# Performance work log

Measured on AMD Instinct MI355X. Metric: run time of the kernel, lower is better.

The kernel has to match this reference:

```python
import jax, jax.numpy as jnp
import numpy as np

B, S, D, H = 2, 2048, 1024, 16
DH = D // H
EPS = 1e-5


def layer_norm(x, g, b):
    # OpenAI-style LN: epsilon inside the sqrt
    u = jnp.mean(x, axis=-1, keepdims=True)
    s = jnp.mean((x - u) ** 2, axis=-1, keepdims=True)
    return g * ((x - u) / jnp.sqrt(s + EPS)) + b


def setup_inputs() -> dict:
    key = jax.random.key(0)
    ks = jax.random.split(key, 8)
    std = 0.002  # Conv1D init std
    return {
        "x": jax.random.normal(ks[0], (B, S, D), dtype=jnp.float32),
        "mask": jnp.ones((B, S), dtype=jnp.bool_),
        "Wqkv": jax.random.normal(ks[1], (D, 3 * D), dtype=jnp.float32) * std,
        "bqkv": jnp.zeros((3 * D,), dtype=jnp.float32),
        "Wvw": jax.random.normal(ks[2], (D, D), dtype=jnp.float32) * std,
        "bvw": jnp.zeros((D,), dtype=jnp.float32),
        "g1": jnp.ones((D,), dtype=jnp.float32),
        "b1": jnp.zeros((D,), dtype=jnp.float32),
        "WA": jax.random.normal(ks[3], (D, 4 * D), dtype=jnp.float32) * std,
        "bA": jnp.zeros((4 * D,), dtype=jnp.float32),
        "WB": jax.random.normal(ks[4], (4 * D, D), dtype=jnp.float32) * std,
        "bB": jnp.zeros((D,), dtype=jnp.float32),
        "g2": jnp.ones((D,), dtype=jnp.float32),
        "b2": jnp.zeros((D,), dtype=jnp.float32),
    }


def reference(x, mask, Wqkv, bqkv, Wvw, bvw, g1, b1, WA, bA, WB, bB, g2, b2):
    maskf = mask.astype(x.dtype)                       # [B,S]
    x = x * maskf[:, :, None]
    # --- multi-head attention ---
    qkv = (x @ Wqkv + bqkv).reshape(B, S, 3, H, DH)    # [B,S,3,H,DH]
    q, k, v = qkv[:, :, 0], qkv[:, :, 1], qkv[:, :, 2]
    w = jnp.einsum('bshd,bzhd->bhsz', q, k) / jnp.sqrt(jnp.asarray(DH, x.dtype))
    causal = jnp.tril(jnp.ones((S, S), dtype=x.dtype)) # [S,S]
    wholemask = maskf[:, None, None, :] * causal[None, None]  # [B,1,S,S]
    w = w + jnp.log(wholemask)                         # additive log-mask (-inf where masked)
    w = jax.nn.softmax(w, axis=-1)
    vw = jnp.einsum('bhsz,bzhd->bshd', w, v).reshape(B, S, D)
    a = vw @ Wvw + bvw
    # --- residual + LN + MLP + LN ---
    n = layer_norm(x + a, g1, b1)
    m = jax.nn.relu(n @ WA + bA) @ WB + bB
    h = layer_norm(n + m, g2, b2)
    return h
```

## Files before the change

### kernel.cpp

```cpp
#include <hip/hip_runtime.h>
#include <stdint.h>

typedef unsigned short u16;
typedef __attribute__((ext_vector_type(8))) short short8;
typedef __attribute__((ext_vector_type(4))) short short4v;
typedef __attribute__((ext_vector_type(4))) float f32x4;

#define NB 2
#define NS 2048
#define ND 1024
#define NH 16
#define NDH 64
#define NBS (NB*NS)

__device__ __forceinline__ float bf2f(u16 u) {
  union { uint32_t i; float f; } c; c.i = ((uint32_t)u) << 16; return c.f;
}
__device__ __forceinline__ u16 f2bf(float f) {
  union { float f; uint32_t i; } c; c.f = f;
  uint32_t r = (c.i + 0x7fffu + ((c.i >> 16) & 1u)) >> 16;
  return (u16)r;
}

__global__ __launch_bounds__(256)
void k_f32_to_bf16(const float* __restrict__ X, u16* __restrict__ Y, int n4) {
  int i = blockIdx.x * 256 + threadIdx.x;
  if (i >= n4) return;
  float4 v = ((const float4*)X)[i];
  uint2 o;
  o.x = (uint32_t)f2bf(v.x) | ((uint32_t)f2bf(v.y) << 16);
  o.y = (uint32_t)f2bf(v.z) | ((uint32_t)f2bf(v.w) << 16);
  ((uint2*)Y)[i] = o;
}

__global__ __launch_bounds__(256)
void k_transpose_all(const float* __restrict__ Wqkv, const float* __restrict__ Wvw,
                     const float* __restrict__ WA, const float* __restrict__ WB,
                     u16* __restrict__ WqkvT, u16* __restrict__ WvwT,
                     u16* __restrict__ WAT, u16* __restrict__ WBT) {
  __shared__ float tile[32][33];
  int id = blockIdx.x;
  const float* W; u16* WT; int K, N, tid;
  if (id < 3072)      { W = Wqkv; WT = WqkvT; K = 1024; N = 3072; tid = id; }
  else if (id < 4096) { W = Wvw;  WT = WvwT;  K = 1024; N = 1024; tid = id - 3072; }
  else if (id < 8192) { W = WA;   WT = WAT;   K = 1024; N = 4096; tid = id - 4096; }
  else                { W = WB;   WT = WBT;   K = 4096; N = 1024; tid = id - 8192; }
  const int ntx = N >> 5;
  const int n0 = (tid % ntx) << 5, k0 = (tid / ntx) << 5;
  const int tx = threadIdx.x & 31, ty = threadIdx.x >> 5;
  #pragma unroll
  for (int j = 0; j < 4; ++j)
    tile[ty + 8*j][tx] = W[(size_t)(k0 + ty + 8*j) * N + (n0 + tx)];
  __syncthreads();
  const int r = threadIdx.x >> 3;
  const int c4 = (threadIdx.x & 7) * 4;
  short4v o;
  #pragma unroll
  for (int i = 0; i < 4; ++i) o[i] = (short)f2bf(tile[c4 + i][r]);
  *(short4v*)(WT + (size_t)(n0 + r) * K + k0 + c4) = o;
}

__global__ __launch_bounds__(256)
void k_vt(const u16* __restrict__ qkv, u16* __restrict__ Vt) {
  __shared__ u16 tile[64][72];
  const int zb = blockIdx.x;
  const int bh = blockIdx.y;
  const int b = bh >> 4, h = bh & 15;
  const int t = threadIdx.x;
  const int r = t >> 2, seg = (t & 3) * 16;
  const u16* src = qkv + ((size_t)(b * NS + zb * 64 + r)) * 3072 + 2048 + h * 64 + seg;
  *(short8*)(&tile[r][seg])     = *(const short8*)(src);
  *(short8*)(&tile[r][seg + 8]) = *(const short8*)(src + 8);
  __syncthreads();
  const int dh = t >> 2, zs = (t & 3) * 16;
  short8 o0, o1;
  #pragma unroll
  for (int i = 0; i < 8; ++i) o0[i] = (short)tile[zs + i][dh];
  #pragma unroll
  for (int i = 0; i < 8; ++i) o1[i] = (short)tile[zs + 8 + i][dh];
  u16* dst = Vt + (size_t)(bh * 64 + dh) * NS + zb * 64 + zs;
  *(short8*)(dst)     = o0;
  *(short8*)(dst + 8) = o1;
}

__device__ __forceinline__ void gload_lds16(const void* g, void* l) {
  __builtin_amdgcn_global_load_lds(
      (const __attribute__((address_space(1))) void*)(void*)(uintptr_t)g,
      (__attribute__((address_space(3))) void*)l, 16, 0, 0);
}

template<bool OUT_BF16, bool RELU>
__global__ __launch_bounds__(256)
void k_gemm_bt(const u16* __restrict__ A, const u16* __restrict__ BT,
               const float* __restrict__ bias, void* __restrict__ C,
               int M, int N, int Kstride, int Klen, size_t zCstride)
{
  __shared__ u16 As[128 * 64];
  __shared__ u16 Bs[128 * 64];
  const int t = threadIdx.x, wave = t >> 6, lane = t & 63;
  const int m0 = blockIdx.y * 128, n0 = blockIdx.x * 128;
  const int wr = wave >> 1, wc = wave & 1;
  const int koff = blockIdx.z * Klen;
  A  += koff;
  BT += koff;

  f32x4 acc[4][4] = {};

  int srow[4], scol[4];
  #pragma unroll
  for (int p = 0; p < 4; ++p) {
    int o = p * 4096 + wave * 1024 + lane * 16;
    int r = o >> 7;
    int cb = o & 127;
    srow[p] = r;
    scol[p] = (cb ^ ((r & 7) << 4)) >> 1;
  }

  const int nkt = Klen >> 6;
  for (int kt = 0; kt < nkt; ++kt) {
    const int k0 = kt << 6;
    #pragma unroll
    for (int p = 0; p < 4; ++p) {
      const u16* srcA = A  + (size_t)(m0 + srow[p]) * Kstride + k0 + scol[p];
      const u16* srcB = BT + (size_t)(n0 + srow[p]) * Kstride + k0 + scol[p];
      gload_lds16(srcA, (char*)As + p * 4096 + wave * 1024);
      gload_lds16(srcB, (char*)Bs + p * 4096 + wave * 1024);
    }
    asm volatile("s_waitcnt vmcnt(0)" ::: "memory");
    __syncthreads();

    #pragma unroll
    for (int kk = 0; kk < 2; ++kk) {
      const int cbase = kk * 64 + ((lane >> 4) << 4);
      short8 af[4], bf[4];
      #pragma unroll
      for (int mi = 0; mi < 4; ++mi) {
        int r = wr * 64 + mi * 16 + (lane & 15);
        af[mi] = *(const short8*)((const char*)As + r * 128 + (cbase ^ ((r & 7) << 4)));
      }
      #pragma unroll
      for (int nj = 0; nj < 4; ++nj) {
        int r = wc * 64 + nj * 16 + (lane & 15);
        bf[nj] = *(const short8*)((const char*)Bs + r * 128 + (cbase ^ ((r & 7) << 4)));
      }
      #pragma unroll
      for (int mi = 0; mi < 4; ++mi)
        #pragma unroll
        for (int nj = 0; nj < 4; ++nj)
          acc[mi][nj] = __builtin_amdgcn_mfma_f32_16x16x32_bf16(af[mi], bf[nj], acc[mi][nj], 0, 0, 0);
    }
    __syncthreads();
  }

  const int lr = (lane >> 4) << 2;
  const int lc = lane & 15;
  #pragma unroll
  for (int nj = 0; nj < 4; ++nj) {
    const int col = n0 + wc * 64 + nj * 16 + lc;
    const float bs = bias ? bias[col] : 0.f;
    #pragma unroll
    for (int mi = 0; mi < 4; ++mi) {
      const int row = m0 + wr * 64 + mi * 16 + lr;
      #pragma unroll
      for (int i = 0; i < 4; ++i) {
        float v = acc[mi][nj][i] + bs;
        if (RELU) v = fmaxf(v, 0.f);
        if (OUT_BF16) ((u16*)C)[blockIdx.z * zCstride + (size_t)(row + i) * N + col] = f2bf(v);
        else          ((float*)C)[blockIdx.z * zCstride + (size_t)(row + i) * N + col] = v;
      }
    }
  }
}

__device__ __forceinline__ short8 lds_frag8(const char* base, int row, int kkbyte) {
  return *(const short8*)(base + row * 128 + (kkbyte ^ ((row & 7) << 4)));
}

template<bool OUT_BF16, bool RELU>
__global__ __launch_bounds__(512, 2)
void k_gemm256(const u16* __restrict__ A, const u16* __restrict__ BT,
               const float* __restrict__ bias, void* __restrict__ C,
               int M, int N, int Kstride, int Klen, int nbx,
               size_t zs1, size_t zs2)
{
  extern __shared__ char lds[];
  char* ldsA = lds;
  char* ldsB = lds + 65536;
  const int t = threadIdx.x, wave = t >> 6, lane = t & 63;
  const int lg = lane >> 4, lq = lane & 15;
  const int wr = wave >> 2, wc = wave & 3;

  const int nwg = gridDim.x;
  const int sw = (blockIdx.x & 7) * (nwg >> 3) + (blockIdx.x >> 3);
  const int bx = sw % nbx, by = sw / nbx;
  const int m0 = by * 256, n0 = bx * 256;

  const int koff = blockIdx.z * Klen;
  A  += koff;
  BT += koff;

  const int rr = t >> 3;
  const int scol = ((t & 7) ^ ((t >> 3) & 7)) * 8;
  const u16* Asrc = A  + (size_t)(m0 + rr) * Kstride + scol;
  const u16* Bsrc = BT + (size_t)(n0 + rr) * Kstride + scol;

  const int nkt = Klen >> 6;
  const int nht = nkt << 2;

  f32x4 acc[8][4] = {};
  short8 af[4][2], bf[4][2];

  auto STAGE = [&](int s) {
    if (s < nht) {
      const int tile = s >> 2, part = s & 3, half = part & 1, slot = tile & 1;
      const u16* src = (part < 2 ? Bsrc : Asrc) + (size_t)(half * 128) * Kstride + tile * 64;
      char* d = (part < 2 ? ldsB : ldsA) + slot * 32768 + half * 16384 + wave * 1024;
      gload_lds16(src, d);
      gload_lds16(src + (size_t)64 * Kstride, d + 8192);
    }
  };
  auto RDA = [&](int slot, int mo) {
    const char* base = ldsA + slot * 32768;
    #pragma unroll
    for (int m = 0; m < 4; ++m) {
      const int row = wr * 128 + (mo + m) * 16 + lq;
      af[m][0] = lds_frag8(base, row, lg * 16);
      af[m][1] = lds_frag8(base, row, 64 + lg * 16);
    }
  };
  auto RDB = [&](int slot, int no) {
    const char* base = ldsB + slot * 32768;
    #pragma unroll
    for (int n = 0; n < 2; ++n) {
      const int row = wc * 64 + (no + n) * 16 + lq;
      bf[no + n][0] = lds_frag8(base, row, lg * 16);
      bf[no + n][1] = lds_frag8(base, row, 64 + lg * 16);
    }
  };
  auto MF = [&](int mo, int no) {
    __builtin_amdgcn_s_setprio(1);
    #pragma unroll
    for (int m = 0; m < 4; ++m)
      #pragma unroll
      for (int n = 0; n < 2; ++n) {
        acc[mo + m][no + n] = __builtin_amdgcn_mfma_f32_16x16x32_bf16(af[m][0], bf[no + n][0], acc[mo + m][no + n], 0, 0, 0);
        acc[mo + m][no + n] = __builtin_amdgcn_mfma_f32_16x16x32_bf16(af[m][1], bf[no + n][1], acc[mo + m][no + n], 0, 0, 0);
      }
    __builtin_amdgcn_s_setprio(0);
  };
  #define BAR() asm volatile("s_barrier" ::: "memory")

  #pragma unroll
  for (int s = 0; s < 6; ++s) STAGE(s);
  asm volatile("s_waitcnt vmcnt(4)" ::: "memory");
  __syncthreads();

  const int niter = nkt >> 1;
  #pragma unroll 1
  for (int i = 0; i < niter; ++i) {
    const int bs = 8 * i + 6;
    RDA(0, 0); RDB(0, 0); STAGE(bs + 0);
    BAR(); MF(0, 0); BAR();
    RDB(0, 2); STAGE(bs + 1);
    BAR(); MF(0, 2); BAR();
    RDA(0, 4); STAGE(bs + 2);
    BAR(); MF(4, 0); BAR();
    STAGE(bs + 3);
    if (i == niter - 1) { asm volatile("s_waitcnt vmcnt(0)" ::: "memory"); }
    else                { asm volatile("s_waitcnt vmcnt(4)" ::: "memory"); }
    BAR(); MF(4, 2); BAR();
    RDA(1, 0); RDB(1, 0); STAGE(bs + 4);
    BAR(); MF(0, 0); BAR();
    RDB(1, 2); STAGE(bs + 5);
    BAR(); MF(0, 2); BAR();
    RDA(1, 4); STAGE(bs + 6);
    BAR(); MF(4, 0); BAR();
    STAGE(bs + 7);
    asm volatile("s_waitcnt vmcnt(4)" ::: "memory");
    BAR(); MF(4, 2); BAR();
  }
  #undef BAR

  const size_t zoff = (size_t)(blockIdx.z & 1) * zs1 + (size_t)(blockIdx.z >> 1) * zs2;
  #pragma unroll
  for (int n = 0; n < 4; ++n) {
    const int col = n0 + wc * 64 + n * 16 + lq;
    const float bs = bias ? bias[col] : 0.f;
    #pragma unroll
    for (int m = 0; m < 8; ++m) {
      const int row = m0 + wr * 128 + m * 16 + lg * 4;
      #pragma unroll
      for (int i = 0; i < 4; ++i) {
        float v = acc[m][n][i] + bs;
        if (RELU) v = fmaxf(v, 0.f);
        if (OUT_BF16) ((u16*)C)[zoff + (size_t)(row + i) * N + col] = f2bf(v);
        else          ((float*)C)[zoff + (size_t)(row + i) * N + col] = v;
      }
    }
  }
}

__global__ __launch_bounds__(512)
void k_flash_attn(const u16* __restrict__ qkv, const u16* __restrict__ Vt,
                  u16* __restrict__ vw)
{
  __shared__ u16 Ks[2][64 * 64];
  __shared__ u16 Vts[2][64 * 64];
  __shared__ u16 P_lds[8][16 * 72];

  const int qb = 15 - (int)blockIdx.x;
  const int bh = blockIdx.y;
  const int b = bh >> 4, h = bh & 15;
  const int t = threadIdx.x, wave = t >> 6, lane = t & 63;
  const int lg = lane >> 4, lq = lane & 15;

  const int q0w = qb * 128 + wave * 16;

  const float QSC = 0.18033688f;
  short8 bq[2];
  {
    const u16* qrow = qkv + ((size_t)(b * NS + q0w + lq)) * 3072 + h * 64 + lg * 8;
    short8 r0 = *(const short8*)(qrow);
    short8 r1 = *(const short8*)(qrow + 32);
    union { short8 s; uint32_t u[4]; } o0, o1;
    #pragma unroll
    for (int p = 0; p < 4; ++p) {
      float a0 = bf2f((u16)r0[2*p]) * QSC, a1 = bf2f((u16)r0[2*p+1]) * QSC;
      float c0 = bf2f((u16)r1[2*p]) * QSC, c1 = bf2f((u16)r1[2*p+1]) * QSC;
      asm("v_cvt_pk_bf16_f32 %0, %1, %2" : "=v"(o0.u[p]) : "v"(a0), "v"(a1));
      asm("v_cvt_pk_bf16_f32 %0, %1, %2" : "=v"(o1.u[p]) : "v"(c0), "v"(c1));
    }
    bq[0] = o0.s; bq[1] = o1.s;
  }

  f32x4 o_acc[4] = {};
  float m_run = -1e30f, l_run = 0.f;

  const u16* kbase = qkv + (size_t)b * NS * 3072 + 1024 + h * 64;
  const u16* vtb   = Vt + (size_t)bh * 64 * NS;

  const int so = t * 16;
  const int sr = so >> 7;
  const int scb = (so & 127) ^ ((sr & 7) << 4);
  const int npairs = qb + 1;

  short8 rK0, rK1, rV0, rV1;
  auto LOADP = [&](int z0) {
    rK0 = *(const short8*)(kbase + (size_t)(z0 + sr) * 3072 + (scb >> 1));
    rK1 = *(const short8*)(kbase + (size_t)(z0 + 64 + sr) * 3072 + (scb >> 1));
    rV0 = *(const short8*)(vtb + (size_t)sr * NS + z0 + (scb >> 1));
    rV1 = *(const short8*)(vtb + (size_t)sr * NS + z0 + 64 + (scb >> 1));
  };

  LOADP(0);

  for (int kp = 0; kp < npairs; ++kp) {
    const int z0 = kp * 128;
    asm volatile("s_waitcnt vmcnt(0)" ::: "memory");
    *(short8*)((char*)Ks[0]  + so) = rK0;
    *(short8*)((char*)Ks[1]  + so) = rK1;
    *(short8*)((char*)Vts[0] + so) = rV0;
    *(short8*)((char*)Vts[1] + so) = rV1;
    if (kp + 1 < npairs) LOADP(z0 + 128);
    asm volatile("s_waitcnt lgkmcnt(0)" ::: "memory");
    asm volatile("s_barrier" ::: "memory");

    #pragma unroll
    for (int sub = 0; sub < 2; ++sub) {
      const int zz = z0 + (sub << 6);
      if (zz <= q0w + 15) {
        f32x4 s_acc[4];
        __builtin_amdgcn_s_setprio(1);
        #pragma unroll
        for (int kb = 0; kb < 4; ++kb) {
          const int r = kb * 16 + lq;
          const int sw = (r & 7) << 4;
          short8 ak0 = *(const short8*)((const char*)Ks[sub] + r * 128 + ((lg * 16) ^ sw));
          short8 ak1 = *(const short8*)((const char*)Ks[sub] + r * 128 + ((64 + lg * 16) ^ sw));
          f32x4 zr = {0.f, 0.f, 0.f, 0.f};
          zr = __builtin_amdgcn_mfma_f32_16x16x32_bf16(ak0, bq[0], zr, 0, 0, 0);
          s_acc[kb] = __builtin_amdgcn_mfma_f32_16x16x32_bf16(ak1, bq[1], zr, 0, 0, 0);
        }
        __builtin_amdgcn_s_setprio(0);

        short8 vb[4][2];
        #pragma unroll
        for (int nb = 0; nb < 4; ++nb) {
          const int rv = nb * 16 + lq;
          const int swv = (rv & 7) << 4;
          vb[nb][0] = *(const short8*)((const char*)Vts[sub] + rv * 128 + ((lg * 16) ^ swv));
          vb[nb][1] = *(const short8*)((const char*)Vts[sub] + rv * 128 + ((64 + lg * 16) ^ swv));
        }

        float sv[16];
        #pragma unroll
        for (int kb = 0; kb < 4; ++kb)
          #pragma unroll
          for (int i = 0; i < 4; ++i)
            sv[kb * 4 + i] = s_acc[kb][i];

        if (zz + 63 > q0w) {
          #pragma unroll
          for (int kb = 0; kb < 4; ++kb)
            #pragma unroll
            for (int i = 0; i < 4; ++i)
              if (zz + kb * 16 + lg * 4 + i > q0w + lq) sv[kb * 4 + i] = -1e30f;
        }

        float tm = -1e30f;
        #pragma unroll
        for (int j = 0; j < 16; ++j) tm = fmaxf(tm, sv[j]);
        tm = fmaxf(tm, __shfl_xor(tm, 16));
        tm = fmaxf(tm, __shfl_xor(tm, 32));

        if (!__all(tm <= m_run + 11.5415603f)) {
          const float m_new = fmaxf(m_run, tm);
          const float scl = __builtin_amdgcn_exp2f(m_run - m_new);
          float s0 = __shfl(scl, lg * 4 + 0);
          float s1 = __shfl(scl, lg * 4 + 1);
          float s2 = __shfl(scl, lg * 4 + 2);
          float s3 = __shfl(scl, lg * 4 + 3);
          #pragma unroll
          for (int nb = 0; nb < 4; ++nb) {
            o_acc[nb][0] *= s0; o_acc[nb][1] *= s1;
            o_acc[nb][2] *= s2; o_acc[nb][3] *= s3;
          }
          l_run *= scl;
          m_run = m_new;
        }

        float ts = 0.f;
        #pragma unroll
        for (int j = 0; j < 16; ++j) {
          float p = __builtin_amdgcn_exp2f(sv[j] - m_run);
          sv[j] = p; ts += p;
        }
        ts += __shfl_xor(ts, 16);
        ts += __shfl_xor(ts, 32);
        l_run += ts;

        #pragma unroll
        for (int kb = 0; kb < 4; ++kb) {
          uint32_t w0, w1;
          asm("v_cvt_pk_bf16_f32 %0, %1, %2" : "=v"(w0) : "v"(sv[kb*4+0]), "v"(sv[kb*4+1]));
          asm("v_cvt_pk_bf16_f32 %0, %1, %2" : "=v"(w1) : "v"(sv[kb*4+2]), "v"(sv[kb*4+3]));
          uint32_t* dst = (uint32_t*)&P_lds[wave][lq * 72 + kb * 16 + lg * 4];
          dst[0] = w0; dst[1] = w1;
        }
        short8 pa0 = *(const short8*)(&P_lds[wave][lq * 72 + lg * 8]);
        short8 pa1 = *(const short8*)(&P_lds[wave][lq * 72 + 32 + lg * 8]);

        __builtin_amdgcn_s_setprio(1);
        #pragma unroll
        for (int nb = 0; nb < 4; ++nb) {
          o_acc[nb] = __builtin_amdgcn_mfma_f32_16x16x32_bf16(pa0, vb[nb][0], o_acc[nb], 0, 0, 0);
          o_acc[nb] = __builtin_amdgcn_mfma_f32_16x16x32_bf16(pa1, vb[nb][1], o_acc[nb], 0, 0, 0);
        }
        __builtin_amdgcn_s_setprio(0);
      }
    }
    asm volatile("s_barrier" ::: "memory");
  }

  #pragma unroll
  for (int i = 0; i < 4; ++i) {
    const float rl = 1.0f / __shfl(l_run, lg * 4 + i);
    const int row = q0w + lg * 4 + i;
    #pragma unroll
    for (int nb = 0; nb < 4; ++nb) {
      const int col = h * 64 + nb * 16 + lq;
      vw[((size_t)b * NS + row) * ND + col] = f2bf(o_acc[nb][i] * rl);
    }
  }
}

__global__ __launch_bounds__(256)
void k_add_ln1s(const float* __restrict__ X, const float* __restrict__ P0,
                const float* __restrict__ P1, const float* __restrict__ bias,
                const float* __restrict__ g, const float* __restrict__ beta,
                float* __restrict__ outf, u16* __restrict__ outb)
{
  const int row = blockIdx.x;
  const int t = threadIdx.x;
  const size_t base = (size_t)row * ND;
  float4 u  = ((const float4*)(X + base))[t];
  float4 p0 = ((const float4*)(P0 + base))[t];
  float4 p1 = ((const float4*)(P1 + base))[t];
  float4 bv = ((const float4*)bias)[t];
  float x0 = u.x + p0.x + p1.x + bv.x;
  float x1 = u.y + p0.y + p1.y + bv.y;
  float x2 = u.z + p0.z + p1.z + bv.z;
  float x3 = u.w + p0.w + p1.w + bv.w;
  float s1 = x0 + x1 + x2 + x3;
  float s2 = x0*x0 + x1*x1 + x2*x2 + x3*x3;
  #pragma unroll
  for (int m = 32; m; m >>= 1) { s1 += __shfl_xor(s1, m); s2 += __shfl_xor(s2, m); }
  __shared__ float rs1[4], rs2[4];
  const int wave = t >> 6;
  if ((t & 63) == 0) { rs1[wave] = s1; rs2[wave] = s2; }
  __syncthreads();
  s1 = rs1[0] + rs1[1] + rs1[2] + rs1[3];
  s2 = rs2[0] + rs2[1] + rs2[2] + rs2[3];
  const float mean = s1 * (1.f / ND);
  const float var  = s2 * (1.f / ND) - mean * mean;
  const float rstd = rsqrtf(var + 1e-5f);
  float4 gg = ((const float4*)g)[t];
  float4 bb = ((const float4*)beta)[t];
  float y0 = gg.x * (x0 - mean) * rstd + bb.x;
  float y1 = gg.y * (x1 - mean) * rstd + bb.y;
  float y2 = gg.z * (x2 - mean) * rstd + bb.z;
  float y3 = gg.w * (x3 - mean) * rstd + bb.w;
  ((float4*)(outf + base))[t] = make_float4(y0, y1, y2, y3);
  uint2 ob;
  ob.x = (uint32_t)f2bf(y0) | ((uint32_t)f2bf(y1) << 16);
  ob.y = (uint32_t)f2bf(y2) | ((uint32_t)f2bf(y3) << 16);
  ((uint2*)(outb + base))[t] = ob;
}

__global__ __launch_bounds__(256)
void k_add_ln2b(const float* __restrict__ U,
                const u16* __restrict__ p0, const u16* __restrict__ p1,
                const u16* __restrict__ p2, const u16* __restrict__ p3,
                const float* __restrict__ bias,
                const float* __restrict__ g, const float* __restrict__ beta,
                float* __restrict__ outf)
{
  const int row = blockIdx.x;
  const int t = threadIdx.x;
  const size_t base = (size_t)row * ND;
  float4 u  = ((const float4*)(U + base))[t];
  float4 bv = ((const float4*)bias)[t];
  uint2 a0 = ((const uint2*)(p0 + base))[t];
  uint2 a1 = ((const uint2*)(p1 + base))[t];
  uint2 a2 = ((const uint2*)(p2 + base))[t];
  uint2 a3 = ((const uint2*)(p3 + base))[t];
  float x0 = u.x + bv.x + bf2f((u16)(a0.x)) + bf2f((u16)(a1.x)) + bf2f((u16)(a2.x)) + bf2f((u16)(a3.x));
  float x1 = u.y + bv.y + bf2f((u16)(a0.x >> 16)) + bf2f((u16)(a1.x >> 16)) + bf2f((u16)(a2.x >> 16)) + bf2f((u16)(a3.x >> 16));
  float x2 = u.z + bv.z + bf2f((u16)(a0.y)) + bf2f((u16)(a1.y)) + bf2f((u16)(a2.y)) + bf2f((u16)(a3.y));
  float x3 = u.w + bv.w + bf2f((u16)(a0.y >> 16)) + bf2f((u16)(a1.y >> 16)) + bf2f((u16)(a2.y >> 16)) + bf2f((u16)(a3.y >> 16));
  float s1 = x0 + x1 + x2 + x3;
  float s2 = x0*x0 + x1*x1 + x2*x2 + x3*x3;
  #pragma unroll
  for (int m = 32; m; m >>= 1) { s1 += __shfl_xor(s1, m); s2 += __shfl_xor(s2, m); }
  __shared__ float rs1[4], rs2[4];
  const int wave = t >> 6;
  if ((t & 63) == 0) { rs1[wave] = s1; rs2[wave] = s2; }
  __syncthreads();
  s1 = rs1[0] + rs1[1] + rs1[2] + rs1[3];
  s2 = rs2[0] + rs2[1] + rs2[2] + rs2[3];
  const float mean = s1 * (1.f / ND);
  const float var  = s2 * (1.f / ND) - mean * mean;
  const float rstd = rsqrtf(var + 1e-5f);
  float4 gg = ((const float4*)g)[t];
  float4 bb = ((const float4*)beta)[t];
  float y0 = gg.x * (x0 - mean) * rstd + bb.x;
  float y1 = gg.y * (x1 - mean) * rstd + bb.y;
  float y2 = gg.z * (x2 - mean) * rstd + bb.z;
  float y3 = gg.w * (x3 - mean) * rstd + bb.w;
  ((float4*)(outf + base))[t] = make_float4(y0, y1, y2, y3);
}

__global__ __launch_bounds__(256)
void k_add_ln2(const float* __restrict__ U, const float* __restrict__ P0,
               const float* __restrict__ P1, const float* __restrict__ bias,
               const float* __restrict__ g, const float* __restrict__ beta,
               float* __restrict__ outf)
{
  const int row = blockIdx.x;
  const int t = threadIdx.x;
  const size_t base = (size_t)row * ND;
  float4 u  = ((const float4*)(U + base))[t];
  float4 p0 = ((const float4*)(P0 + base))[t];
  float4 p1 = ((const float4*)(P1 + base))[t];
  float4 bv = ((const float4*)bias)[t];
  float x0 = u.x + p0.x + p1.x + bv.x;
  float x1 = u.y + p0.y + p1.y + bv.y;
  float x2 = u.z + p0.z + p1.z + bv.z;
  float x3 = u.w + p0.w + p1.w + bv.w;
  float s1 = x0 + x1 + x2 + x3;
  float s2 = x0*x0 + x1*x1 + x2*x2 + x3*x3;
  #pragma unroll
  for (int m = 32; m; m >>= 1) { s1 += __shfl_xor(s1, m); s2 += __shfl_xor(s2, m); }
  __shared__ float rs1[4], rs2[4];
  const int wave = t >> 6;
  if ((t & 63) == 0) { rs1[wave] = s1; rs2[wave] = s2; }
  __syncthreads();
  s1 = rs1[0] + rs1[1] + rs1[2] + rs1[3];
  s2 = rs2[0] + rs2[1] + rs2[2] + rs2[3];
  const float mean = s1 * (1.f / ND);
  const float var  = s2 * (1.f / ND) - mean * mean;
  const float rstd = rsqrtf(var + 1e-5f);
  float4 gg = ((const float4*)g)[t];
  float4 bb = ((const float4*)beta)[t];
  float y0 = gg.x * (x0 - mean) * rstd + bb.x;
  float y1 = gg.y * (x1 - mean) * rstd + bb.y;
  float y2 = gg.z * (x2 - mean) * rstd + bb.z;
  float y3 = gg.w * (x3 - mean) * rstd + bb.w;
  ((float4*)(outf + base))[t] = make_float4(y0, y1, y2, y3);
}

extern "C" void kernel_launch(void* const* d_in, const int* in_sizes, int n_in,
                              void* d_out, int out_size, void* d_ws, size_t ws_size,
                              hipStream_t stream) {
  const float* x    = (const float*)d_in[0];
  const float* Wqkv = (const float*)d_in[2];
  const float* bqkv = (const float*)d_in[3];
  const float* Wvw  = (const float*)d_in[4];
  const float* bvw  = (const float*)d_in[5];
  const float* g1   = (const float*)d_in[6];
  const float* b1   = (const float*)d_in[7];
  const float* WA   = (const float*)d_in[8];
  const float* bA   = (const float*)d_in[9];
  const float* WB   = (const float*)d_in[10];
  const float* bB   = (const float*)d_in[11];
  const float* g2   = (const float*)d_in[12];
  const float* b2   = (const float*)d_in[13];
  float* out = (float*)d_out;

  if (ws_size < 100663296) return;
  char* ws = (char*)d_ws;
  u16*  WqkvT = (u16*)(ws + 0);
  u16*  WvwT  = (u16*)(ws + 6291456);
  u16*  WAT   = (u16*)(ws + 8388608);
  u16*  WBT   = (u16*)(ws + 16777216);
  u16*  xb    = (u16*)(ws + 25165824);
  u16*  qkvb  = (u16*)(ws + 33554432);
  u16*  vwb   = (u16*)(ws + 58720256);
  float* pp0  = (float*)(ws + 67108864);
  float* pp1  = (float*)(ws + 83886080);
  float* nf   = (float*)(ws + 83886080);
  u16*  nb    = (u16*)(ws + 25165824);
  u16*  z     = (u16*)(ws + 33554432);
  u16*  Vtb   = (u16*)(ws + 67108864);
  u16*  pb01  = (u16*)(ws + 0);
  u16*  pb23  = (u16*)(ws + 67108864);
  float* pp   = (float*)ws;

  hipError_t e2 = hipFuncSetAttribute((const void*)&k_gemm256<true, true>,
                                      hipFuncAttributeMaxDynamicSharedMemorySize, 131072);
  hipError_t e1 = hipFuncSetAttribute((const void*)&k_gemm256<true, false>,
                                      hipFuncAttributeMaxDynamicSharedMemorySize, 131072);
  const bool use256 = (e1 == hipSuccess) && (e2 == hipSuccess);

  k_f32_to_bf16<<<dim3(NBS * ND / 4 / 256), 256, 0, stream>>>(x, xb, NBS * ND / 4);
  k_transpose_all<<<dim3(12288), 256, 0, stream>>>(Wqkv, Wvw, WA, WB, WqkvT, WvwT, WAT, WBT);

  k_gemm_bt<true, false><<<dim3(3 * ND / 128, NBS / 128, 1), 256, 0, stream>>>(
      xb, WqkvT, bqkv, qkvb, NBS, 3 * ND, ND, ND, 0);

  k_vt<<<dim3(NS / 64, NB * NH), 256, 0, stream>>>(qkvb, Vtb);
  k_flash_attn<<<dim3(NS / 128, NB * NH), 512, 0, stream>>>(qkvb, Vtb, vwb);

  k_gemm_bt<false, false><<<dim3(ND / 128, NBS / 128, 2), 256, 0, stream>>>(
      vwb, WvwT, nullptr, pp0, NBS, ND, ND, ND / 2, (size_t)(pp1 - pp0));

  k_add_ln1s<<<dim3(NBS), 256, 0, stream>>>(x, pp0, pp1, bvw, g1, b1, nf, nb);

  if (use256)
    k_gemm256<true, true><<<dim3(256), 512, 131072, stream>>>(
        nb, WAT, bA, z, NBS, 4 * ND, ND, ND, 16, 0, 0);
  else
    k_gemm_bt<true, true><<<dim3(4 * ND / 128, NBS / 128, 1), 256, 0, stream>>>(
        nb, WAT, bA, z, NBS, 4 * ND, ND, ND, 0);

  if (use256) {
    k_gemm256<true, false><<<dim3(64, 1, 4), 512, 131072, stream>>>(
        z, WBT, nullptr, pb01, NBS, ND, 4 * ND, ND, 4,
        (size_t)4194304, (size_t)(pb23 - pb01));
    k_add_ln2b<<<dim3(NBS), 256, 0, stream>>>(
        nf, pb01, pb01 + 4194304, pb23, pb23 + 4194304, bB, g2, b2, out);
  } else {
    k_gemm_bt<false, false><<<dim3(ND / 128, NBS / 128, 2), 256, 0, stream>>>(
        z, WBT, nullptr, pp, NBS, ND, 4 * ND, 2 * ND, (size_t)16777216);
    k_add_ln2<<<dim3(NBS), 256, 0, stream>>>(nf, pp, pp + 16777216, bB, g2, b2, out);
  }
}
```

Baseline: 232.2 us.

## Merge prep kernels, halve attention block size, store split-K partials in bf16

Combines the x-to-bf16 conversion and weight transpose into one prep launch. The flash attention kernel now uses 64-query blocks of 4 waves, which doubles the grid. Each thread stages twice as much K/V data per iteration. The Wvw split-K partials are written as bf16 instead of fp32 to cut traffic into LN1, at some precision cost. The fallback MLP path now uses four bf16 partials and the shared LN2b kernel.

```diff
diff --git a/kernel.cpp b/kernel.cpp
--- a/kernel.cpp
+++ b/kernel.cpp
@@ -23,23 +23,22 @@
 }
 
 __global__ __launch_bounds__(256)
-void k_f32_to_bf16(const float* __restrict__ X, u16* __restrict__ Y, int n4) {
-  int i = blockIdx.x * 256 + threadIdx.x;
-  if (i >= n4) return;
-  float4 v = ((const float4*)X)[i];
-  uint2 o;
-  o.x = (uint32_t)f2bf(v.x) | ((uint32_t)f2bf(v.y) << 16);
-  o.y = (uint32_t)f2bf(v.z) | ((uint32_t)f2bf(v.w) << 16);
-  ((uint2*)Y)[i] = o;
-}
-
-__global__ __launch_bounds__(256)
-void k_transpose_all(const float* __restrict__ Wqkv, const float* __restrict__ Wvw,
-                     const float* __restrict__ WA, const float* __restrict__ WB,
-                     u16* __restrict__ WqkvT, u16* __restrict__ WvwT,
-                     u16* __restrict__ WAT, u16* __restrict__ WBT) {
+void k_prep(const float* __restrict__ x, u16* __restrict__ xb,
+            const float* __restrict__ Wqkv, const float* __restrict__ Wvw,
+            const float* __restrict__ WA, const float* __restrict__ WB,
+            u16* __restrict__ WqkvT, u16* __restrict__ WvwT,
+            u16* __restrict__ WAT, u16* __restrict__ WBT) {
   __shared__ float tile[32][33];
   int id = blockIdx.x;
+  if (id >= 12288) {
+    int i = (id - 12288) * 256 + threadIdx.x;
+    float4 v = ((const float4*)x)[i];
+    uint2 o;
+    o.x = (uint32_t)f2bf(v.x) | ((uint32_t)f2bf(v.y) << 16);
+    o.y = (uint32_t)f2bf(v.z) | ((uint32_t)f2bf(v.w) << 16);
+    ((uint2*)xb)[i] = o;
+    return;
+  }
   const float* W; u16* WT; int K, N, tid;
   if (id < 3072)      { W = Wqkv; WT = WqkvT; K = 1024; N = 3072; tid = id; }
   else if (id < 4096) { W = Wvw;  WT = WvwT;  K = 1024; N = 1024; tid = id - 3072; }
@@ -300,21 +299,21 @@
   }
 }
 
-__global__ __launch_bounds__(512)
+__global__ __launch_bounds__(256)
 void k_flash_attn(const u16* __restrict__ qkv, const u16* __restrict__ Vt,
                   u16* __restrict__ vw)
 {
   __shared__ u16 Ks[2][64 * 64];
   __shared__ u16 Vts[2][64 * 64];
-  __shared__ u16 P_lds[8][16 * 72];
-
-  const int qb = 15 - (int)blockIdx.x;
+  __shared__ u16 P_lds[4][16 * 72];
+
+  const int qb = 31 - (int)blockIdx.x;
   const int bh = blockIdx.y;
   const int b = bh >> 4, h = bh & 15;
   const int t = threadIdx.x, wave = t >> 6, lane = t & 63;
   const int lg = lane >> 4, lq = lane & 15;
 
-  const int q0w = qb * 128 + wave * 16;
+  const int q0w = qb * 64 + wave * 16;
 
   const float QSC = 0.18033688f;
   short8 bq[2];
@@ -339,17 +338,27 @@
   const u16* kbase = qkv + (size_t)b * NS * 3072 + 1024 + h * 64;
   const u16* vtb   = Vt + (size_t)bh * 64 * NS;
 
-  const int so = t * 16;
+  const int so = t * 32;
   const int sr = so >> 7;
-  const int scb = (so & 127) ^ ((sr & 7) << 4);
-  const int npairs = qb + 1;
-
-  short8 rK0, rK1, rV0, rV1;
+  const int cb = so & 127;
+  const int swz = (sr & 7) << 4;
+  const int sc0 = (cb ^ swz) >> 1;
+  const int sc1 = ((cb + 16) ^ swz) >> 1;
+  const int npairs = (qb >> 1) + 1;
+
+  short8 rg[8];
   auto LOADP = [&](int z0) {
-    rK0 = *(const short8*)(kbase + (size_t)(z0 + sr) * 3072 + (scb >> 1));
-    rK1 = *(const short8*)(kbase + (size_t)(z0 + 64 + sr) * 3072 + (scb >> 1));
-    rV0 = *(const short8*)(vtb + (size_t)sr * NS + z0 + (scb >> 1));
-    rV1 = *(const short8*)(vtb + (size_t)sr * NS + z0 + 64 + (scb >> 1));
+    const u16* k0 = kbase + (size_t)(z0 + sr) * 3072;
+    const u16* k1 = kbase + (size_t)(z0 + 64 + sr) * 3072;
+    const u16* v0 = vtb + (size_t)sr * NS + z0;
+    rg[0] = *(const short8*)(k0 + sc0);
+    rg[1] = *(const short8*)(k0 + sc1);
+    rg[2] = *(const short8*)(k1 + sc0);
+    rg[3] = *(const short8*)(k1 + sc1);
+    rg[4] = *(const short8*)(v0 + sc0);
+    rg[5] = *(const short8*)(v0 + sc1);
+    rg[6] = *(const short8*)(v0 + 64 + sc0);
+    rg[7] = *(const short8*)(v0 + 64 + sc1);
   };
 
   LOADP(0);
@@ -357,10 +366,14 @@
   for (int kp = 0; kp < npairs; ++kp) {
     const int z0 = kp * 128;
     asm volatile("s_waitcnt vmcnt(0)" ::: "memory");
-    *(short8*)((char*)Ks[0]  + so) = rK0;
-    *(short8*)((char*)Ks[1]  + so) = rK1;
-    *(short8*)((char*)Vts[0] + so) = rV0;
-    *(short8*)((char*)Vts[1] + so) = rV1;
+    *(short8*)((char*)Ks[0]  + so)      = rg[0];
+    *(short8*)((char*)Ks[0]  + so + 16) = rg[1];
+    *(short8*)((char*)Ks[1]  + so)      = rg[2];
+    *(short8*)((char*)Ks[1]  + so + 16) = rg[3];
+    *(short8*)((char*)Vts[0] + so)      = rg[4];
+    *(short8*)((char*)Vts[0] + so + 16) = rg[5];
+    *(short8*)((char*)Vts[1] + so)      = rg[6];
+    *(short8*)((char*)Vts[1] + so + 16) = rg[7];
     if (kp + 1 < npairs) LOADP(z0 + 128);
     asm volatile("s_waitcnt lgkmcnt(0)" ::: "memory");
     asm volatile("s_barrier" ::: "memory");
@@ -475,8 +488,8 @@
 }
 
 __global__ __launch_bounds__(256)
-void k_add_ln1s(const float* __restrict__ X, const float* __restrict__ P0,
-                const float* __restrict__ P1, const float* __restrict__ bias,
+void k_add_ln1s(const float* __restrict__ X, const u16* __restrict__ P0,
+                const u16* __restrict__ P1, const float* __restrict__ bias,
                 const float* __restrict__ g, const float* __restrict__ beta,
                 float* __restrict__ outf, u16* __restrict__ outb)
 {
@@ -484,13 +497,13 @@
   const int t = threadIdx.x;
   const size_t base = (size_t)row * ND;
   float4 u  = ((const float4*)(X + base))[t];
-  float4 p0 = ((const float4*)(P0 + base))[t];
-  float4 p1 = ((const float4*)(P1 + base))[t];
+  uint2 a0 = ((const uint2*)(P0 + base))[t];
+  uint2 a1 = ((const uint2*)(P1 + base))[t];
   float4 bv = ((const float4*)bias)[t];
-  float x0 = u.x + p0.x + p1.x + bv.x;
-  float x1 = u.y + p0.y + p1.y + bv.y;
-  float x2 = u.z + p0.z + p1.z + bv.z;
-  float x3 = u.w + p0.w + p1.w + bv.w;
+  float x0 = u.x + bv.x + bf2f((u16)(a0.x)) + bf2f((u16)(a1.x));
+  float x1 = u.y + bv.y + bf2f((u16)(a0.x >> 16)) + bf2f((u16)(a1.x >> 16));
+  float x2 = u.z + bv.z + bf2f((u16)(a0.y)) + bf2f((u16)(a1.y));
+  float x3 = u.w + bv.w + bf2f((u16)(a0.y >> 16)) + bf2f((u16)(a1.y >> 16));
   float s1 = x0 + x1 + x2 + x3;
   float s2 = x0*x0 + x1*x1 + x2*x2 + x3*x3;
   #pragma unroll
@@ -560,45 +573,6 @@
   ((float4*)(outf + base))[t] = make_float4(y0, y1, y2, y3);
 }
 
-__global__ __launch_bounds__(256)
-void k_add_ln2(const float* __restrict__ U, const float* __restrict__ P0,
-               const float* __restrict__ P1, const float* __restrict__ bias,
-               const float* __restrict__ g, const float* __restrict__ beta,
-               float* __restrict__ outf)
-{
-  const int row = blockIdx.x;
-  const int t = threadIdx.x;
-  const size_t base = (size_t)row * ND;
-  float4 u  = ((const float4*)(U + base))[t];
-  float4 p0 = ((const float4*)(P0 + base))[t];
-  float4 p1 = ((const float4*)(P1 + base))[t];
-  float4 bv = ((const float4*)bias)[t];
-  float x0 = u.x + p0.x + p1.x + bv.x;
-  float x1 = u.y + p0.y + p1.y + bv.y;
-  float x2 = u.z + p0.z + p1.z + bv.z;
-  float x3 = u.w + p0.w + p1.w + bv.w;
-  float s1 = x0 + x1 + x2 + x3;
-  float s2 = x0*x0 + x1*x1 + x2*x2 + x3*x3;
-  #pragma unroll
-  for (int m = 32; m; m >>= 1) { s1 += __shfl_xor(s1, m); s2 += __shfl_xor(s2, m); }
-  __shared__ float rs1[4], rs2[4];
-  const int wave = t >> 6;
-  if ((t & 63) == 0) { rs1[wave] = s1; rs2[wave] = s2; }
-  __syncthreads();
-  s1 = rs1[0] + rs1[1] + rs1[2] + rs1[3];
-  s2 = rs2[0] + rs2[1] + rs2[2] + rs2[3];
-  const float mean = s1 * (1.f / ND);
-  const float var  = s2 * (1.f / ND) - mean * mean;
-  const float rstd = rsqrtf(var + 1e-5f);
-  float4 gg = ((const float4*)g)[t];
-  float4 bb = ((const float4*)beta)[t];
-  float y0 = gg.x * (x0 - mean) * rstd + bb.x;
-  float y1 = gg.y * (x1 - mean) * rstd + bb.y;
-  float y2 = gg.z * (x2 - mean) * rstd + bb.z;
-  float y3 = gg.w * (x3 - mean) * rstd + bb.w;
-  ((float4*)(outf + base))[t] = make_float4(y0, y1, y2, y3);
-}
-
 extern "C" void kernel_launch(void* const* d_in, const int* in_sizes, int n_in,
                               void* d_out, int out_size, void* d_ws, size_t ws_size,
                               hipStream_t stream) {
@@ -626,15 +600,14 @@
   u16*  xb    = (u16*)(ws + 25165824);
   u16*  qkvb  = (u16*)(ws + 33554432);
   u16*  vwb   = (u16*)(ws + 58720256);
-  float* pp0  = (float*)(ws + 67108864);
-  float* pp1  = (float*)(ws + 83886080);
+  u16*  po0   = (u16*)(ws + 67108864);
+  u16*  po1   = (u16*)(ws + 75497472);
   float* nf   = (float*)(ws + 83886080);
   u16*  nb    = (u16*)(ws + 25165824);
   u16*  z     = (u16*)(ws + 33554432);
   u16*  Vtb   = (u16*)(ws + 67108864);
   u16*  pb01  = (u16*)(ws + 0);
   u16*  pb23  = (u16*)(ws + 67108864);
-  float* pp   = (float*)ws;
 
   hipError_t e2 = hipFuncSetAttribute((const void*)&k_gemm256<true, true>,
                                       hipFuncAttributeMaxDynamicSharedMemorySize, 131072);
@@ -642,19 +615,18 @@
                                       hipFuncAttributeMaxDynamicSharedMemorySize, 131072);
   const bool use256 = (e1 == hipSuccess) && (e2 == hipSuccess);
 
-  k_f32_to_bf16<<<dim3(NBS * ND / 4 / 256), 256, 0, stream>>>(x, xb, NBS * ND / 4);
-  k_transpose_all<<<dim3(12288), 256, 0, stream>>>(Wqkv, Wvw, WA, WB, WqkvT, WvwT, WAT, WBT);
+  k_prep<<<dim3(16384), 256, 0, stream>>>(x, xb, Wqkv, Wvw, WA, WB, WqkvT, WvwT, WAT, WBT);
 
   k_gemm_bt<true, false><<<dim3(3 * ND / 128, NBS / 128, 1), 256, 0, stream>>>(
       xb, WqkvT, bqkv, qkvb, NBS, 3 * ND, ND, ND, 0);
 
   k_vt<<<dim3(NS / 64, NB * NH), 256, 0, stream>>>(qkvb, Vtb);
-  k_flash_attn<<<dim3(NS / 128, NB * NH), 512, 0, stream>>>(qkvb, Vtb, vwb);
-
-  k_gemm_bt<false, false><<<dim3(ND / 128, NBS / 128, 2), 256, 0, stream>>>(
-      vwb, WvwT, nullptr, pp0, NBS, ND, ND, ND / 2, (size_t)(pp1 - pp0));
-
-  k_add_ln1s<<<dim3(NBS), 256, 0, stream>>>(x, pp0, pp1, bvw, g1, b1, nf, nb);
+  k_flash_attn<<<dim3(NS / 64, NB * NH), 256, 0, stream>>>(qkvb, Vtb, vwb);
+
+  k_gemm_bt<true, false><<<dim3(ND / 128, NBS / 128, 2), 256, 0, stream>>>(
+      vwb, WvwT, nullptr, po0, NBS, ND, ND, ND / 2, (size_t)(po1 - po0));
+
+  k_add_ln1s<<<dim3(NBS), 256, 0, stream>>>(x, po0, po1, bvw, g1, b1, nf, nb);
 
   if (use256)
     k_gemm256<true, true><<<dim3(256), 512, 131072, stream>>>(
@@ -670,8 +642,10 @@
     k_add_ln2b<<<dim3(NBS), 256, 0, stream>>>(
         nf, pb01, pb01 + 4194304, pb23, pb23 + 4194304, bB, g2, b2, out);
   } else {
-    k_gemm_bt<false, false><<<dim3(ND / 128, NBS / 128, 2), 256, 0, stream>>>(
-        z, WBT, nullptr, pp, NBS, ND, 4 * ND, 2 * ND, (size_t)16777216);
-    k_add_ln2<<<dim3(NBS), 256, 0, stream>>>(nf, pp, pp + 16777216, bB, g2, b2, out);
-  }
-}
+    k_gemm_bt<true, false><<<dim3(ND / 128, NBS / 128, 4), 256, 0, stream>>>(
+        z, WBT, nullptr, pb01, NBS, ND, 4 * ND, ND, (size_t)4194304);
+    k_add_ln2b<<<dim3(NBS), 256, 0, stream>>>(
+        nf, pb01, pb01 + 4194304, pb01 + 2 * 4194304, pb01 + 3 * 4194304,
+        bB, g2, b2, out);
+  }
+}
```

Result: slower. 251.7 us (+8.4%).
